# Kernel tuning notes

Hardware: AMD Instinct MI355X
Metric: run time of the kernel (lower is better)

## Reference

```python
import jax, jax.numpy as jnp
import numpy as np

N_NODES = 100000
N_EDGES = 3200000
N_FEAT = 128


def setup_inputs() -> dict:
    key = jax.random.key(0)
    ks = jax.random.split(key, 8)
    x = jax.random.normal(ks[0], (N_NODES, N_FEAT), dtype=jnp.float32)
    edge_index = jax.random.randint(ks[1], (2, N_EDGES), 0, N_NODES, dtype=jnp.int64)

    def glorot(k, fan_in, fan_out):
        s = (6.0 / (fan_in + fan_out)) ** 0.5
        return jax.random.uniform(k, (fan_in, fan_out), jnp.float32, -s, s)

    return {
        "x": x,
        "edge_index": edge_index,
        "W1": glorot(ks[2], N_FEAT, 64), "b1": jnp.zeros((64,), jnp.float32),
        "W2": glorot(ks[3], 64, 32),     "b2": jnp.zeros((32,), jnp.float32),
        "W3": glorot(ks[4], 32, 2),      "b3": jnp.zeros((2,), jnp.float32),
    }


def _gcn_norm(edge_index, num_nodes):
    # Add self loops, then symmetric normalization D^{-1/2} (A+I) D^{-1/2}
    loop = jnp.arange(num_nodes, dtype=edge_index.dtype)
    src = jnp.concatenate([edge_index[0], loop])
    dst = jnp.concatenate([edge_index[1], loop])
    deg = jax.ops.segment_sum(jnp.ones_like(dst, dtype=jnp.float32), dst,
                              num_segments=num_nodes)
    dinv = jnp.where(deg > 0, jax.lax.rsqrt(deg), 0.0)
    norm = dinv[src] * dinv[dst]  # [E + N]
    return src, dst, norm


def _gcn_conv(h, W, b, src, dst, norm, num_nodes):
    h = h @ W  # small dense GEMM
    msg = h[src] * norm[:, None]  # gather + scale
    out = jax.ops.segment_sum(msg, dst, num_segments=num_nodes)  # scatter-add
    return out + b


def reference(x, edge_index, W1, b1, W2, b2, W3, b3):
    n = x.shape[0]
    src, dst, norm = _gcn_norm(edge_index, n)
    h = jax.nn.relu(_gcn_conv(x, W1, b1, src, dst, norm, n))
    # dropout(p=0.5) is identity in eval mode
    h = jax.nn.relu(_gcn_conv(h, W2, b2, src, dst, norm, n))
    h = _gcn_conv(h, W3, b3, src, dst, norm, n)
    return jax.nn.log_softmax(h, axis=1)
```

## Files before the change

kernel.cpp:

```cpp
#include <hip/hip_runtime.h>
#include <math.h>

#define EPB 8192
#define CAP 10240
#define MAXB 16384

typedef __attribute__((ext_vector_type(8))) short bf16x8;
typedef __attribute__((ext_vector_type(4))) float f32x4;
typedef __attribute__((ext_vector_type(2))) float f32x2;


__device__ inline unsigned short f2b(float f) {
  union { float f; unsigned u; } c; c.f = f;
  unsigned r = c.u + 0x7fff + ((c.u >> 16) & 1);
  return (unsigned short)(r >> 16);
}


__global__ __launch_bounds__(256) void k_bscan2(const int* __restrict__ cnts, int* __restrict__ bbase,
                                                int* __restrict__ rowptr, int E, int N, int NBKT) {
  __shared__ int a[512], c[512];
  int tid = threadIdx.x;
  int v0 = (tid < NBKT) ? cnts[tid] : 0;
  int v1 = (tid + 256 < NBKT) ? cnts[tid + 256] : 0;
  a[tid] = v0; a[tid + 256] = v1;
  __syncthreads();
  int* pin = a; int* pout = c;
  for (int st = 1; st < 512; st <<= 1) {
    pout[tid]       = pin[tid]       + ((tid >= st)       ? pin[tid - st]       : 0);
    pout[tid + 256] = pin[tid + 256] + ((tid + 256 >= st) ? pin[tid + 256 - st] : 0);
    __syncthreads();
    int* t = pin; pin = pout; pout = t;
  }
  if (tid < NBKT)       bbase[tid] = pin[tid] - v0;
  if (tid + 256 < NBKT) bbase[tid + 256] = pin[tid + 256] - v1;
  if (tid == 0) { bbase[NBKT] = E; rowptr[N] = E; }
}


__global__ __launch_bounds__(512) void k_bucket_scatter(const int* __restrict__ src, const int* __restrict__ dst,
                                                        int* __restrict__ gcur, unsigned* __restrict__ tmp,
                                                        int E, int NBKT) {
  __shared__ int hist[512], base[512], loff[512];
  __shared__ int sa[512], sc[512];
  __shared__ unsigned stage[EPB];
  __shared__ unsigned short bkt16[EPB];
  int tid = threadIdx.x;
  int ebeg = blockIdx.x * EPB;
  int eend = min(E, ebeg + EPB);
  hist[tid] = 0;
  __syncthreads();
  int e0 = ebeg + tid * 16;
  int nE = eend - e0; if (nE < 0) nE = 0; if (nE > 16) nE = 16;
  int d[16], s[16], rk[16];
  if (nE == 16) {
#pragma unroll
    for (int q = 0; q < 4; ++q) {
      int4 dv = *(const int4*)(dst + e0 + q * 4);
      int4 sv = *(const int4*)(src + e0 + q * 4);
      d[q * 4 + 0] = dv.x; d[q * 4 + 1] = dv.y; d[q * 4 + 2] = dv.z; d[q * 4 + 3] = dv.w;
      s[q * 4 + 0] = sv.x; s[q * 4 + 1] = sv.y; s[q * 4 + 2] = sv.z; s[q * 4 + 3] = sv.w;
    }
  } else {
#pragma unroll
    for (int k = 0; k < 16; ++k) {
      if (k < nE) { d[k] = dst[e0 + k]; s[k] = src[e0 + k]; } else { d[k] = 0; s[k] = 0; }
    }
  }
#pragma unroll
  for (int k = 0; k < 16; ++k) rk[k] = (k < nE) ? atomicAdd(&hist[d[k] >> 8], 1) : 0;
  __syncthreads();
  int hc = hist[tid];
  sa[tid] = hc;
  base[tid] = (tid < NBKT && hc) ? atomicAdd(&gcur[tid], hc) : 0;
  __syncthreads();
  int* pin = sa; int* pout = sc;
  for (int st = 1; st < 512; st <<= 1) {
    pout[tid] = pin[tid] + ((tid >= st) ? pin[tid - st] : 0);
    __syncthreads();
    int* t = pin; pin = pout; pout = t;
  }
  loff[tid] = pin[tid] - hc;
  __syncthreads();
#pragma unroll
  for (int k = 0; k < 16; ++k) if (k < nE) {
    int bkt = d[k] >> 8;
    int pos = loff[bkt] + rk[k];
    stage[pos] = ((unsigned)s[k] << 8) | (unsigned)(d[k] & 255);
    bkt16[pos] = (unsigned short)bkt;
  }
  __syncthreads();
  int cnt = eend - ebeg;
  for (int k = tid; k < cnt; k += 512) {
    int b = bkt16[k];
    tmp[(size_t)b * CAP + base[b] + (k - loff[b])] = stage[k];
  }
}


__global__ __launch_bounds__(512) void k_bucket_build(const unsigned* __restrict__ tmp, const int* __restrict__ cnts,
                                                      const int* __restrict__ bbase, int* __restrict__ csr,
                                                      int* __restrict__ rowptr, float* __restrict__ dinv, int N) {
  int b = blockIdx.x;
  int tid = threadIdx.x;
  int node0 = b << 8;
  int nn = min(256, N - node0);
  int cnt = cnts[b];
  int gbeg = bbase[b];
  const unsigned* tb = tmp + (size_t)b * CAP;
  __shared__ int h[256], off[256], cur[256];
  __shared__ unsigned short rk[MAXB];
  __shared__ int stage[MAXB];
  if (tid < 256) h[tid] = 0;
  __syncthreads();
  bool fast = (cnt <= MAXB);
  if (fast) {
    for (int e = tid; e < cnt; e += 512) {
      unsigned p = tb[e];
      rk[e] = (unsigned short)atomicAdd(&h[p & 255], 1);
    }
  } else {
    for (int e = tid; e < cnt; e += 512) atomicAdd(&h[tb[e] & 255], 1);
  }
  __syncthreads();
  int deg = 0;
  if (tid < 256) { deg = h[tid]; off[tid] = deg; }
  __syncthreads();
  for (int st = 1; st < 256; st <<= 1) {
    int t = 0;
    if (tid < 256 && tid >= st) t = off[tid - st];
    __syncthreads();
    if (tid < 256) off[tid] += t;
    __syncthreads();
  }
  if (tid < 256) {
    int excl = off[tid] - deg;
    cur[tid] = excl;
    if (tid < nn) {
      rowptr[node0 + tid] = gbeg + excl;
      dinv[node0 + tid] = rsqrtf((float)(deg + 1));
    }
  }
  __syncthreads();
  if (fast) {
    for (int e = tid; e < cnt; e += 512) {
      unsigned p = tb[e];
      stage[cur[p & 255] + (int)rk[e]] = (int)(p >> 8);
    }
    __syncthreads();
    for (int k = tid; k < cnt; k += 512) csr[gbeg + k] = stage[k];
  } else {
    for (int e = tid; e < cnt; e += 512) {
      unsigned p = tb[e];
      int pos = atomicAdd(&cur[p & 255], 1);
      csr[gbeg + pos] = (int)(p >> 8);
    }
  }
}


template <int F_IN, int F_OUT>
__global__ __launch_bounds__(256) void k_gemm_mfma(const float* __restrict__ x, const float* __restrict__ W,
                                                   const float* __restrict__ dinv, unsigned short* __restrict__ g,
                                                   int N, int NT) {
  constexpr int NKS = F_IN / 32;
  constexpr int NCT = F_OUT / 16;
  int tid = threadIdx.x;
  int w = tid >> 6, lane = tid & 63;
  int lo = lane & 15, hi = lane >> 4;

  union U8 { bf16x8 v; unsigned u[4]; };
  U8 bf[NCT][NKS];
#pragma unroll
  for (int ct = 0; ct < NCT; ++ct)
#pragma unroll
    for (int ks = 0; ks < NKS; ++ks) {
      const float* wp = W + (size_t)(ks * 32 + hi * 8) * F_OUT + ct * 16 + lo;
      float f[8];
#pragma unroll
      for (int j = 0; j < 8; ++j) f[j] = wp[(size_t)j * F_OUT];
#pragma unroll
      for (int j = 0; j < 4; ++j)
        asm("v_cvt_pk_bf16_f32 %0, %1, %2" : "=v"(bf[ct][ks].u[j]) : "v"(f[2 * j]), "v"(f[2 * j + 1]));
    }

  for (int t = blockIdx.x * 4 + w; t < NT; t += gridDim.x * 4) {
    int row0 = t << 4;
    f32x4 acc[NCT];
#pragma unroll
    for (int ct = 0; ct < NCT; ++ct) acc[ct] = (f32x4){0.f, 0.f, 0.f, 0.f};
    int rl = row0 + lo; if (rl >= N) rl = N - 1;
    const float* xrow = x + (size_t)rl * F_IN;
#pragma unroll
    for (int ks = 0; ks < NKS; ++ks) {
      const float* xp = xrow + ks * 32 + hi * 8;
      float4 a0 = *(const float4*)xp;
      float4 a1 = *(const float4*)(xp + 4);
      U8 af;
      asm("v_cvt_pk_bf16_f32 %0, %1, %2" : "=v"(af.u[0]) : "v"(a0.x), "v"(a0.y));
      asm("v_cvt_pk_bf16_f32 %0, %1, %2" : "=v"(af.u[1]) : "v"(a0.z), "v"(a0.w));
      asm("v_cvt_pk_bf16_f32 %0, %1, %2" : "=v"(af.u[2]) : "v"(a1.x), "v"(a1.y));
      asm("v_cvt_pk_bf16_f32 %0, %1, %2" : "=v"(af.u[3]) : "v"(a1.z), "v"(a1.w));
#pragma unroll
      for (int ct = 0; ct < NCT; ++ct)
        acc[ct] = __builtin_amdgcn_mfma_f32_16x16x32_bf16(af.v, bf[ct][ks].v, acc[ct], 0, 0, 0);
    }
    float dvv[4];
    if (row0 + 16 <= N) {
      float4 d4 = *(const float4*)(dinv + row0 + (hi << 2));
      dvv[0] = d4.x; dvv[1] = d4.y; dvv[2] = d4.z; dvv[3] = d4.w;
    } else {
#pragma unroll
      for (int j = 0; j < 4; ++j) { int r = row0 + (hi << 2) + j; dvv[j] = dinv[r < N ? r : N - 1]; }
    }
#pragma unroll
    for (int ct = 0; ct < NCT; ++ct) {
#pragma unroll
      for (int j = 0; j < 4; ++j) {
        int row = row0 + (hi << 2) + j;
        if (row < N) g[(size_t)row * F_OUT + ct * 16 + lo] = f2b(dvv[j] * acc[ct][j]);
      }
    }
  }
}


template <int F_IN, int F_OUT, int TPN, int ROWS>
__global__ __launch_bounds__(256) void k_gemm(const float* __restrict__ x, const float* __restrict__ W,
                                              const float* __restrict__ dinv, unsigned short* __restrict__ g, int N) {
  constexpr int VPT = F_OUT / TPN;
  constexpr int GROUPS = 256 / TPN;
  constexpr int NB = GROUPS * ROWS;
  __shared__ float ws[F_IN * F_OUT];
  __shared__ float xs[NB][F_IN];
  int tid = threadIdx.x;
  int base = blockIdx.x * NB;
  for (int i = tid; i < F_IN * F_OUT; i += 256) ws[i] = W[i];
  for (int i = tid; i < NB * F_IN; i += 256) {
    int r = i / F_IN, c = i - r * F_IN;
    int node = base + r;
    xs[r][c ^ (r & 31)] = (node < N) ? x[(size_t)node * F_IN + c] : 0.f;
  }
  __syncthreads();
  int fg = tid % TPN, f0 = fg * VPT;
  int ng = tid / TPN;
  int r0 = ng * ROWS;
  float acc[ROWS][VPT];
#pragma unroll
  for (int r = 0; r < ROWS; ++r)
#pragma unroll
    for (int j = 0; j < VPT; ++j) acc[r][j] = 0.f;
  for (int k = 0; k < F_IN; ++k) {
    float wv[VPT];
#pragma unroll
    for (int j = 0; j < VPT; ++j) wv[j] = ws[k * F_OUT + f0 + j];
#pragma unroll
    for (int r = 0; r < ROWS; ++r) {
      float xv = xs[r0 + r][k ^ ((r0 + r) & 31)];
#pragma unroll
      for (int j = 0; j < VPT; ++j) acc[r][j] += xv * wv[j];
    }
  }
#pragma unroll
  for (int r = 0; r < ROWS; ++r) {
    int node = base + r0 + r;
    if (node < N) {
      float dv = dinv[node];
#pragma unroll
      for (int j = 0; j < VPT; ++j) g[(size_t)node * F_OUT + f0 + j] = f2b(dv * acc[r][j]);
    }
  }
}


#define ACC2(vv) acc0 += __uint_as_float((vv) << 16); acc1 += __uint_as_float((vv) & 0xffff0000u)

template <int FOUT, bool RELU>
__global__ __launch_bounds__(256) void k_agg_full(const unsigned short* __restrict__ g,
                                                  const int* __restrict__ rowptr, const int* __restrict__ csr,
                                                  const float* __restrict__ dinv, const float* __restrict__ bias,
                                                  float* __restrict__ out, int N) {
  constexpr int LSH = (FOUT == 64) ? 5 : 4;
  constexpr int RSH = (FOUT == 64) ? 7 : 6;
  int t = blockIdx.x * 256 + threadIdx.x;
  int grp = t >> LSH;
  if (grp >= N) return;
  unsigned subB = ((unsigned)t & ((1u << LSH) - 1u)) << 2;
  const char* gb = (const char*)g;
  auto gat = [&](int sid) -> unsigned {
    return *(const unsigned*)(gb + ((((unsigned)sid) << RSH) + subB));
  };
  unsigned u = gat(grp);
  float acc0 = __uint_as_float(u << 16);
  float acc1 = __uint_as_float(u & 0xffff0000u);
  int beg = rowptr[grp], end = rowptr[grp + 1];
  int j = beg;
  for (; j < end && (j & 3); ++j) {
    unsigned v = gat(csr[j]); ACC2(v);
  }
  for (; j + 16 <= end; j += 16) {
    int4 sA = *(const int4*)(csr + j);
    int4 sB = *(const int4*)(csr + j + 4);
    int4 sC = *(const int4*)(csr + j + 8);
    int4 sD = *(const int4*)(csr + j + 12);
    unsigned v0 = gat(sA.x), v1 = gat(sA.y), v2 = gat(sA.z), v3 = gat(sA.w);
    unsigned v4 = gat(sB.x), v5 = gat(sB.y), v6 = gat(sB.z), v7 = gat(sB.w);
    unsigned v8 = gat(sC.x), v9 = gat(sC.y), vA = gat(sC.z), vB = gat(sC.w);
    unsigned vC = gat(sD.x), vD = gat(sD.y), vE = gat(sD.z), vF = gat(sD.w);
    ACC2(v0); ACC2(v1); ACC2(v2); ACC2(v3);
    ACC2(v4); ACC2(v5); ACC2(v6); ACC2(v7);
    ACC2(v8); ACC2(v9); ACC2(vA); ACC2(vB);
    ACC2(vC); ACC2(vD); ACC2(vE); ACC2(vF);
  }
  if (j + 8 <= end) {
    int4 sA = *(const int4*)(csr + j);
    int4 sB = *(const int4*)(csr + j + 4);
    unsigned v0 = gat(sA.x), v1 = gat(sA.y), v2 = gat(sA.z), v3 = gat(sA.w);
    unsigned v4 = gat(sB.x), v5 = gat(sB.y), v6 = gat(sB.z), v7 = gat(sB.w);
    ACC2(v0); ACC2(v1); ACC2(v2); ACC2(v3);
    ACC2(v4); ACC2(v5); ACC2(v6); ACC2(v7);
    j += 8;
  }
  if (j + 4 <= end) {
    int4 sA = *(const int4*)(csr + j);
    unsigned v0 = gat(sA.x), v1 = gat(sA.y), v2 = gat(sA.z), v3 = gat(sA.w);
    ACC2(v0); ACC2(v1); ACC2(v2); ACC2(v3);
    j += 4;
  }
  for (; j < end; ++j) {
    unsigned v = gat(csr[j]); ACC2(v);
  }
  float dv = dinv[grp];
  int fg = (int)(subB >> 1);
  float r0 = fmaf(dv, acc0, bias[fg]);
  float r1 = fmaf(dv, acc1, bias[fg + 1]);
  if (RELU) { r0 = fmaxf(r0, 0.f); r1 = fmaxf(r1, 0.f); }
  *(float2*)(out + (size_t)grp * FOUT + fg) = make_float2(r0, r1);
}


__global__ __launch_bounds__(256) void k_final(const unsigned* __restrict__ g2, const int* __restrict__ rowptr,
                                               const int* __restrict__ csr, const float* __restrict__ dinv,
                                               const float* __restrict__ bias, float* __restrict__ out, int N) {
  int i = blockIdx.x * 256 + threadIdx.x;
  if (i >= N) return;
  const char* gb = (const char*)g2;
  unsigned s = *(const unsigned*)(gb + (((unsigned)i) << 2));
  float a0 = __uint_as_float(s << 16), a1 = __uint_as_float(s & 0xffff0000u);
  int beg = rowptr[i], end = rowptr[i + 1];
  int j = beg;
  for (; j < end && (j & 3); ++j) {
    unsigned p = *(const unsigned*)(gb + (((unsigned)csr[j]) << 2));
    a0 += __uint_as_float(p << 16);
    a1 += __uint_as_float(p & 0xffff0000u);
  }
  for (; j + 4 <= end; j += 4) {
    int4 ss = *(const int4*)(csr + j);
    unsigned p0 = *(const unsigned*)(gb + (((unsigned)ss.x) << 2));
    unsigned p1 = *(const unsigned*)(gb + (((unsigned)ss.y) << 2));
    unsigned p2 = *(const unsigned*)(gb + (((unsigned)ss.z) << 2));
    unsigned p3 = *(const unsigned*)(gb + (((unsigned)ss.w) << 2));
    a0 += __uint_as_float(p0 << 16); a1 += __uint_as_float(p0 & 0xffff0000u);
    a0 += __uint_as_float(p1 << 16); a1 += __uint_as_float(p1 & 0xffff0000u);
    a0 += __uint_as_float(p2 << 16); a1 += __uint_as_float(p2 & 0xffff0000u);
    a0 += __uint_as_float(p3 << 16); a1 += __uint_as_float(p3 & 0xffff0000u);
  }
  for (; j < end; ++j) {
    unsigned p = *(const unsigned*)(gb + (((unsigned)csr[j]) << 2));
    a0 += __uint_as_float(p << 16);
    a1 += __uint_as_float(p & 0xffff0000u);
  }
  float dv = dinv[i];
  float v0 = fmaf(dv, a0, bias[0]);
  float v1 = fmaf(dv, a1, bias[1]);
  float m = fmaxf(v0, v1);
  float lse = m + logf(expf(v0 - m) + expf(v1 - m));
  f32x2 o; o.x = v0 - lse; o.y = v1 - lse;
  __builtin_nontemporal_store(o, (f32x2*)(out + 2 * (size_t)i));
}


extern "C" void kernel_launch(void* const* d_in, const int* in_sizes, int n_in,
                              void* d_out, int out_size, void* d_ws, size_t ws_size,
                              hipStream_t stream) {
  const float* x  = (const float*)d_in[0];
  const int*   ei = (const int*)d_in[1];
  const float* W1 = (const float*)d_in[2];
  const float* b1 = (const float*)d_in[3];
  const float* W2 = (const float*)d_in[4];
  const float* b2 = (const float*)d_in[5];
  const float* W3 = (const float*)d_in[6];
  const float* b3 = (const float*)d_in[7];
  float* out = (float*)d_out;

  int N = in_sizes[0] / 128;
  int E = in_sizes[1] / 2;
  const int* src = ei;
  const int* dst = ei + E;
  int NBKT = (N + 255) >> 8;
  int NT = (N + 15) / 16;

  char* w = (char*)d_ws;
  size_t off = 0;
  auto carve = [&](size_t bytes) -> char* {
    char* p = w + off;
    off = (off + bytes + 255) & ~(size_t)255;
    return p;
  };
  float* dinv   = (float*)carve((size_t)N * 4);
  int*   rowptr = (int*)carve((size_t)(N + 1) * 4);
  int*   bbase  = (int*)carve(2048 + 4);
  int*   gcur   = (int*)carve(2048);
  int*   csr    = (int*)carve((size_t)E * 4);
  size_t gsz = (size_t)N * 64 * 2;
  size_t capb = (size_t)NBKT * CAP * 4;
  if (capb > gsz) gsz = capb;
  unsigned short* gbuf = (unsigned short*)carve(gsz);
  float* hbuf   = (float*)carve((size_t)N * 64 * 4);
  unsigned* tmp = (unsigned*)gbuf;
  (void)ws_size; (void)n_in; (void)out_size;

  (void)hipMemsetAsync(gcur, 0, 2048, stream);
  k_bucket_scatter<<<(E + EPB - 1) / EPB, 512, 0, stream>>>(src, dst, gcur, tmp, E, NBKT);
  k_bscan2<<<1, 256, 0, stream>>>(gcur, bbase, rowptr, E, N, NBKT);
  k_bucket_build<<<NBKT, 512, 0, stream>>>(tmp, gcur, bbase, csr, rowptr, dinv, N);

  k_gemm_mfma<128, 64><<<782, 256, 0, stream>>>(x, W1, dinv, gbuf, N, NT);
  k_agg_full<64, true><<<(unsigned)(((long long)N * 32 + 255) / 256), 256, 0, stream>>>(gbuf, rowptr, csr, dinv, b1, hbuf, N);
  k_gemm_mfma<64, 32><<<782, 256, 0, stream>>>(hbuf, W2, dinv, gbuf, N, NT);
  k_agg_full<32, true><<<(unsigned)(((long long)N * 16 + 255) / 256), 256, 0, stream>>>(gbuf, rowptr, csr, dinv, b2, hbuf, N);
  k_gemm<32, 2, 1, 1><<<(N + 255) / 256, 256, 0, stream>>>(hbuf, W3, dinv, gbuf, N);
  k_final<<<(unsigned)((N + 255) / 256), 256, 0, stream>>>((const unsigned*)gbuf, rowptr, csr, dinv, b3, out, N);
}
```

Measured before the change: 214.0 us.

## Fuse layer-2 aggregation with layer-3 GEMM and shrink bucket-scatter block size

Replaces the separate layer-2 aggregation and the tiny 32x2 GEMM with one kernel. It applies bias and ReLU, multiplies by W3 using a 16-lane shuffle reduction, and writes the bf16 pair directly. This removes a full 32-wide fp32 write and re-read of the hidden buffer and one kernel launch. It also halves the edges handled per bucket-scatter block (more blocks, less shared memory) and shrinks the bucket-build shared arrays to CAP, which may raise occupancy.

Result: faster. 201.5 us (-5.8%).

```diff
diff --git a/kernel.cpp b/kernel.cpp
--- a/kernel.cpp
+++ b/kernel.cpp
@@ -1,9 +1,8 @@
 #include <hip/hip_runtime.h>
 #include <math.h>
 
-#define EPB 8192
+#define EPB 4096
 #define CAP 10240
-#define MAXB 16384
 
 typedef __attribute__((ext_vector_type(8))) short bf16x8;
 typedef __attribute__((ext_vector_type(4))) float f32x4;
@@ -50,12 +49,12 @@
   int eend = min(E, ebeg + EPB);
   hist[tid] = 0;
   __syncthreads();
-  int e0 = ebeg + tid * 16;
-  int nE = eend - e0; if (nE < 0) nE = 0; if (nE > 16) nE = 16;
-  int d[16], s[16], rk[16];
-  if (nE == 16) {
-#pragma unroll
-    for (int q = 0; q < 4; ++q) {
+  int e0 = ebeg + tid * 8;
+  int nE = eend - e0; if (nE < 0) nE = 0; if (nE > 8) nE = 8;
+  int d[8], s[8], rk[8];
+  if (nE == 8) {
+#pragma unroll
+    for (int q = 0; q < 2; ++q) {
       int4 dv = *(const int4*)(dst + e0 + q * 4);
       int4 sv = *(const int4*)(src + e0 + q * 4);
       d[q * 4 + 0] = dv.x; d[q * 4 + 1] = dv.y; d[q * 4 + 2] = dv.z; d[q * 4 + 3] = dv.w;
@@ -63,12 +62,12 @@
     }
   } else {
 #pragma unroll
-    for (int k = 0; k < 16; ++k) {
+    for (int k = 0; k < 8; ++k) {
       if (k < nE) { d[k] = dst[e0 + k]; s[k] = src[e0 + k]; } else { d[k] = 0; s[k] = 0; }
     }
   }
 #pragma unroll
-  for (int k = 0; k < 16; ++k) rk[k] = (k < nE) ? atomicAdd(&hist[d[k] >> 8], 1) : 0;
+  for (int k = 0; k < 8; ++k) rk[k] = (k < nE) ? atomicAdd(&hist[d[k] >> 8], 1) : 0;
   __syncthreads();
   int hc = hist[tid];
   sa[tid] = hc;
@@ -83,7 +82,7 @@
   loff[tid] = pin[tid] - hc;
   __syncthreads();
 #pragma unroll
-  for (int k = 0; k < 16; ++k) if (k < nE) {
+  for (int k = 0; k < 8; ++k) if (k < nE) {
     int bkt = d[k] >> 8;
     int pos = loff[bkt] + rk[k];
     stage[pos] = ((unsigned)s[k] << 8) | (unsigned)(d[k] & 255);
@@ -109,11 +108,11 @@
   int gbeg = bbase[b];
   const unsigned* tb = tmp + (size_t)b * CAP;
   __shared__ int h[256], off[256], cur[256];
-  __shared__ unsigned short rk[MAXB];
-  __shared__ int stage[MAXB];
+  __shared__ unsigned short rk[CAP];
+  __shared__ int stage[CAP];
   if (tid < 256) h[tid] = 0;
   __syncthreads();
-  bool fast = (cnt <= MAXB);
+  bool fast = (cnt <= CAP);
   if (fast) {
     for (int e = tid; e < cnt; e += 512) {
       unsigned p = tb[e];
@@ -220,54 +219,6 @@
         int row = row0 + (hi << 2) + j;
         if (row < N) g[(size_t)row * F_OUT + ct * 16 + lo] = f2b(dvv[j] * acc[ct][j]);
       }
-    }
-  }
-}
-
-
-template <int F_IN, int F_OUT, int TPN, int ROWS>
-__global__ __launch_bounds__(256) void k_gemm(const float* __restrict__ x, const float* __restrict__ W,
-                                              const float* __restrict__ dinv, unsigned short* __restrict__ g, int N) {
-  constexpr int VPT = F_OUT / TPN;
-  constexpr int GROUPS = 256 / TPN;
-  constexpr int NB = GROUPS * ROWS;
-  __shared__ float ws[F_IN * F_OUT];
-  __shared__ float xs[NB][F_IN];
-  int tid = threadIdx.x;
-  int base = blockIdx.x * NB;
-  for (int i = tid; i < F_IN * F_OUT; i += 256) ws[i] = W[i];
-  for (int i = tid; i < NB * F_IN; i += 256) {
-    int r = i / F_IN, c = i - r * F_IN;
-    int node = base + r;
-    xs[r][c ^ (r & 31)] = (node < N) ? x[(size_t)node * F_IN + c] : 0.f;
-  }
-  __syncthreads();
-  int fg = tid % TPN, f0 = fg * VPT;
-  int ng = tid / TPN;
-  int r0 = ng * ROWS;
-  float acc[ROWS][VPT];
-#pragma unroll
-  for (int r = 0; r < ROWS; ++r)
-#pragma unroll
-    for (int j = 0; j < VPT; ++j) acc[r][j] = 0.f;
-  for (int k = 0; k < F_IN; ++k) {
-    float wv[VPT];
-#pragma unroll
-    for (int j = 0; j < VPT; ++j) wv[j] = ws[k * F_OUT + f0 + j];
-#pragma unroll
-    for (int r = 0; r < ROWS; ++r) {
-      float xv = xs[r0 + r][k ^ ((r0 + r) & 31)];
-#pragma unroll
-      for (int j = 0; j < VPT; ++j) acc[r][j] += xv * wv[j];
-    }
-  }
-#pragma unroll
-  for (int r = 0; r < ROWS; ++r) {
-    int node = base + r0 + r;
-    if (node < N) {
-      float dv = dinv[node];
-#pragma unroll
-      for (int j = 0; j < VPT; ++j) g[(size_t)node * F_OUT + f0 + j] = f2b(dv * acc[r][j]);
     }
   }
 }
@@ -339,6 +290,74 @@
 }
 
 
+__global__ __launch_bounds__(256) void k_agg2f(const unsigned short* __restrict__ g,
+                                               const int* __restrict__ rowptr, const int* __restrict__ csr,
+                                               const float* __restrict__ dinv, const float* __restrict__ b2,
+                                               const float* __restrict__ W3, unsigned* __restrict__ g2, int N) {
+  int t = blockIdx.x * 256 + threadIdx.x;
+  int grp = t >> 4;
+  if (grp >= N) return;
+  unsigned subB = ((unsigned)t & 15u) << 2;
+  const char* gb = (const char*)g;
+  auto gat = [&](int sid) -> unsigned {
+    return *(const unsigned*)(gb + ((((unsigned)sid) << 6) + subB));
+  };
+  unsigned u = gat(grp);
+  float acc0 = __uint_as_float(u << 16);
+  float acc1 = __uint_as_float(u & 0xffff0000u);
+  int beg = rowptr[grp], end = rowptr[grp + 1];
+  int j = beg;
+  for (; j < end && (j & 3); ++j) {
+    unsigned v = gat(csr[j]); ACC2(v);
+  }
+  for (; j + 16 <= end; j += 16) {
+    int4 sA = *(const int4*)(csr + j);
+    int4 sB = *(const int4*)(csr + j + 4);
+    int4 sC = *(const int4*)(csr + j + 8);
+    int4 sD = *(const int4*)(csr + j + 12);
+    unsigned v0 = gat(sA.x), v1 = gat(sA.y), v2 = gat(sA.z), v3 = gat(sA.w);
+    unsigned v4 = gat(sB.x), v5 = gat(sB.y), v6 = gat(sB.z), v7 = gat(sB.w);
+    unsigned v8 = gat(sC.x), v9 = gat(sC.y), vA = gat(sC.z), vB = gat(sC.w);
+    unsigned vC = gat(sD.x), vD = gat(sD.y), vE = gat(sD.z), vF = gat(sD.w);
+    ACC2(v0); ACC2(v1); ACC2(v2); ACC2(v3);
+    ACC2(v4); ACC2(v5); ACC2(v6); ACC2(v7);
+    ACC2(v8); ACC2(v9); ACC2(vA); ACC2(vB);
+    ACC2(vC); ACC2(vD); ACC2(vE); ACC2(vF);
+  }
+  if (j + 8 <= end) {
+    int4 sA = *(const int4*)(csr + j);
+    int4 sB = *(const int4*)(csr + j + 4);
+    unsigned v0 = gat(sA.x), v1 = gat(sA.y), v2 = gat(sA.z), v3 = gat(sA.w);
+    unsigned v4 = gat(sB.x), v5 = gat(sB.y), v6 = gat(sB.z), v7 = gat(sB.w);
+    ACC2(v0); ACC2(v1); ACC2(v2); ACC2(v3);
+    ACC2(v4); ACC2(v5); ACC2(v6); ACC2(v7);
+    j += 8;
+  }
+  if (j + 4 <= end) {
+    int4 sA = *(const int4*)(csr + j);
+    unsigned v0 = gat(sA.x), v1 = gat(sA.y), v2 = gat(sA.z), v3 = gat(sA.w);
+    ACC2(v0); ACC2(v1); ACC2(v2); ACC2(v3);
+    j += 4;
+  }
+  for (; j < end; ++j) {
+    unsigned v = gat(csr[j]); ACC2(v);
+  }
+  float dv = dinv[grp];
+  int fg = (int)(subB >> 1);
+  float r0 = fmaxf(fmaf(dv, acc0, b2[fg]), 0.f);
+  float r1 = fmaxf(fmaf(dv, acc1, b2[fg + 1]), 0.f);
+  float4 wv = *(const float4*)(W3 + subB);
+  float p0 = r0 * wv.x + r1 * wv.z;
+  float p1 = r0 * wv.y + r1 * wv.w;
+#pragma unroll
+  for (int m = 1; m < 16; m <<= 1) { p0 += __shfl_xor(p0, m); p1 += __shfl_xor(p1, m); }
+  if ((t & 15) == 0) {
+    unsigned uo = (unsigned)f2b(dv * p0) | ((unsigned)f2b(dv * p1) << 16);
+    g2[grp] = uo;
+  }
+}
+
+
 __global__ __launch_bounds__(256) void k_final(const unsigned* __restrict__ g2, const int* __restrict__ rowptr,
                                                const int* __restrict__ csr, const float* __restrict__ dinv,
                                                const float* __restrict__ bias, float* __restrict__ out, int N) {
@@ -428,7 +447,7 @@
   k_gemm_mfma<128, 64><<<782, 256, 0, stream>>>(x, W1, dinv, gbuf, N, NT);
   k_agg_full<64, true><<<(unsigned)(((long long)N * 32 + 255) / 256), 256, 0, stream>>>(gbuf, rowptr, csr, dinv, b1, hbuf, N);
   k_gemm_mfma<64, 32><<<782, 256, 0, stream>>>(hbuf, W2, dinv, gbuf, N, NT);
-  k_agg_full<32, true><<<(unsigned)(((long long)N * 16 + 255) / 256), 256, 0, stream>>>(gbuf, rowptr, csr, dinv, b2, hbuf, N);
-  k_gemm<32, 2, 1, 1><<<(N + 255) / 256, 256, 0, stream>>>(hbuf, W3, dinv, gbuf, N);
-  k_final<<<(unsigned)((N + 255) / 256), 256, 0, stream>>>((const unsigned*)gbuf, rowptr, csr, dinv, b3, out, N);
-}
+  unsigned* g2 = (unsigned*)hbuf;
+  k_agg2f<<<(unsigned)(((long long)N * 16 + 255) / 256), 256, 0, stream>>>(gbuf, rowptr, csr, dinv, b2, W3, g2, N);
+  k_final<<<(unsigned)((N + 255) / 256), 256, 0, stream>>>(g2, rowptr, csr, dinv, b3, out, N);
+}
```
